# Kernel tuning notes

Measured on AMD Instinct MI355X. Metric: run time of the kernel, lower is better.

## Reference

```python
import math
import jax, jax.numpy as jnp
import numpy as np

B, C, H, W = 8, 512, 32, 32
HEADS = 8


def _mix_rot(re, im, Wm, phi):
    # nn.Linear(dim, dim, bias=False) applied channelwise on [B,C,H,W]:
    # y = x @ Wm.T  ->  einsum over input channel c, output channel d
    re2 = jnp.einsum('bchw,dc->bdhw', re, Wm)
    im2 = jnp.einsum('bchw,dc->bdhw', im, Wm)
    c = jnp.cos(phi)[None, :, None, None]
    s = jnp.sin(phi)[None, :, None, None]
    # complex multiply (re2 + i*im2) * (cos phi + i*sin phi)
    return re2 * c - im2 * s, re2 * s + im2 * c


def setup_inputs() -> dict:
    key = jax.random.key(0)
    ks = jax.random.split(key, 6)
    scale = 1.0 / math.sqrt(C)
    return {
        'z_re': jax.random.normal(ks[0], (B, C, H, W), jnp.float32),
        'z_im': jax.random.normal(ks[1], (B, C, H, W), jnp.float32),
        'Wq': jax.random.normal(ks[2], (C, C), jnp.float32) * scale,
        'phi_q': jnp.zeros((C,), jnp.float32),
        'Wk': jax.random.normal(ks[3], (C, C), jnp.float32) * scale,
        'phi_k': jnp.zeros((C,), jnp.float32),
        'Wv': jax.random.normal(ks[4], (C, C), jnp.float32) * scale,
        'phi_v': jnp.zeros((C,), jnp.float32),
        'Wo': jax.random.normal(ks[5], (C, C), jnp.float32) * scale,
        'phi_o': jnp.zeros((C,), jnp.float32),
    }


def reference(z_re, z_im, Wq, phi_q, Wk, phi_k, Wv, phi_v, Wo, phi_o):
    b, c, h, w = z_re.shape
    T = h * w
    dh = c // HEADS

    def tok(a):  # [B,C,H,W] -> [B,T,C]
        return a.reshape(b, c, T).transpose(0, 2, 1)

    qre, qim = _mix_rot(z_re, z_im, Wq, phi_q)
    kre, kim = _mix_rot(z_re, z_im, Wk, phi_k)
    vre, vim = _mix_rot(z_re, z_im, Wv, phi_v)
    qre, qim = tok(qre), tok(qim)
    kre, kim = tok(kre), tok(kim)
    vre, vim = tok(vre), tok(vim)

    # real part of complex inner product: sums over FULL channel dim (no head split)
    scores = (jnp.einsum('btc,buc->btu', qre, kre)
              + jnp.einsum('btc,buc->btu', qim, kim)) / math.sqrt(dh)
    causal = jnp.triu(jnp.ones((T, T), bool), k=1)
    scores = jnp.where(causal[None], -jnp.inf, scores)
    attn = jax.nn.softmax(scores, axis=-1)

    out_re = jnp.einsum('btu,buc->btc', attn, vre)
    out_im = jnp.einsum('btu,buc->btc', attn, vim)

    def grid(a):  # [B,T,C] -> [B,C,H,W]
        return a.transpose(0, 2, 1).reshape(b, c, h, w)

    return _mix_rot(grid(out_re), grid(out_im), Wo, phi_o)
```

## Files before the change

kernel.cpp:

```cpp
#include <hip/hip_runtime.h>
#include <math.h>

#define NB 8
#define NC 512
#define NT 1024
#define BT (NB * NT)
#define SCALE 0.125f
#define NEG_BIG (-3.0e38f)

typedef __attribute__((ext_vector_type(8))) short short8v;
typedef __attribute__((ext_vector_type(8))) _Float16 half8v;
typedef __attribute__((ext_vector_type(4))) float float4v;
#define MFMA_BF16(A, B, C) __builtin_amdgcn_mfma_f32_16x16x32_bf16(A, B, C, 0, 0, 0)
#define MFMA_F16(A, B, C)  __builtin_amdgcn_mfma_f32_16x16x32_f16(A, B, C, 0, 0, 0)

__device__ __forceinline__ ushort f2bf(float f) {
    union { float f; unsigned int i; } v; v.f = f;
    unsigned int r = v.i + 0x7FFFu + ((v.i >> 16) & 1u);
    return (ushort)(r >> 16);
}

__device__ __forceinline__ ushort f2h(float f) {
    return __builtin_bit_cast(unsigned short, (_Float16)f);
}

__device__ __forceinline__ half8v scale8(short8v raw, float s) {
    half8v h = __builtin_bit_cast(half8v, raw);
    const _Float16 hs = (_Float16)s;
    half8v r;
    #pragma unroll
    for (int q = 0; q < 8; ++q) r[q] = h[q] * hs;
    return r;
}

#if defined(__has_builtin)
#if __has_builtin(__builtin_amdgcn_global_load_lds)
#define HAS_GLDS 1
#endif
#endif

#ifdef HAS_GLDS
__device__ __forceinline__ void glds16(const ushort* g, ushort* l) {
    __builtin_amdgcn_global_load_lds(
        (const __attribute__((address_space(1))) unsigned int*)g,
        (__attribute__((address_space(3))) unsigned int*)l, 16, 0, 0);
}
#endif

template<int ROWS>
__device__ __forceinline__ void stage64(const ushort* __restrict__ g, int rsShorts,
                                        ushort* tile, int w, int lane) {
    const int r8 = lane >> 3;
    const int ck = (lane & 7) ^ r8;
    const ushort* gl = g + (size_t)r8 * rsShorts + (ck << 3);
    constexpr int ni = ROWS / 32;
    #pragma unroll
    for (int s = 0; s < ni; ++s) {
        const int issue = w * ni + s;
#ifdef HAS_GLDS
        glds16(gl + (size_t)issue * 8 * rsShorts, tile + issue * 512);
#else
        const uint4 v = *(const uint4*)(gl + (size_t)issue * 8 * rsShorts);
        *(uint4*)(tile + issue * 512 + lane * 8) = v;
#endif
    }
}

__device__ __forceinline__ short8v frag(const ushort* tile, int rr, int q) {
    return *(const short8v*)(tile + rr * 64 + ((q ^ (rr & 7)) << 3));
}

__device__ __forceinline__ int xcd_swz(int flat, int cpx) {
    return (flat & 7) * cpx + (flat >> 3);
}

__global__ __launch_bounds__(256) void prep_zw_kernel(
    const float* __restrict__ zre, const float* __restrict__ zim,
    ushort* __restrict__ Z,
    const float* __restrict__ Wq, const float* __restrict__ Wk,
    const float* __restrict__ Wv, const float* __restrict__ Wo,
    ushort* __restrict__ Wbf)
{
    const int bx = blockIdx.x;
    const int tid = threadIdx.x;
    if (bx >= 2048) {
        const int idx = (bx - 2048) * 256 + tid;
        const int e4 = idx << 2;
        const int m = e4 >> 18;
        const int off = e4 & ((1 << 18) - 1);
        const float* Ws[4] = {Wq, Wk, Wv, Wo};
        const float4 v = *(const float4*)(Ws[m] + off);
        ushort4 o;
        o.x = f2bf(v.x); o.y = f2bf(v.y); o.z = f2bf(v.z); o.w = f2bf(v.w);
        *(ushort4*)(Wbf + ((size_t)m << 18) + off) = o;
        return;
    }
    const int t0 = (bx & 15) << 6, c0 = ((bx >> 4) & 7) << 6;
    const int bz = bx >> 7, b = bz & 7, comp = bz >> 3;
    const float* src = (comp ? zim : zre) + (size_t)b * NC * NT;
    ushort* dst = Z + (size_t)(comp * NB + b) * NT * NC;

    __shared__ ushort T[64][72];
    #pragma unroll
    for (int r = 0; r < 4; ++r) {
        const int cl = (tid >> 4) + r * 16;
        const int t4 = (tid & 15) << 2;
        const float4 v = *(const float4*)(src + (size_t)(c0 + cl) * NT + t0 + t4);
        T[t4 + 0][cl] = f2bf(v.x); T[t4 + 1][cl] = f2bf(v.y);
        T[t4 + 2][cl] = f2bf(v.z); T[t4 + 3][cl] = f2bf(v.w);
    }
    __syncthreads();
    const int tl = tid >> 2, cc = (tid & 3) << 4;
    ushort* op = dst + (size_t)(t0 + tl) * NC + c0 + cc;
    *(uint4*)op       = *(const uint4*)&T[tl][cc];
    *(uint4*)(op + 8) = *(const uint4*)&T[tl][cc + 8];
}

__global__ __launch_bounds__(256, 2) void proj_qk_kernel(
    const ushort* __restrict__ Z, const ushort* __restrict__ Wbf,
    const float* __restrict__ phiq, const float* __restrict__ phik,
    ushort* __restrict__ qre, ushort* __restrict__ qim,
    ushort* __restrict__ kre, ushort* __restrict__ kim)
{
    const int tid = threadIdx.x;
    const int swz = xcd_swz(blockIdx.x + 64 * blockIdx.y, 64);
    const int d0 = (swz & 7) << 6;
    const int m0 = (swz >> 3) << 7;
    const size_t NE = (size_t)BT * NC;

    __shared__ alignas(16) ushort SM[24576];
    ushort* Zr   = SM;
    ushort* Zi   = SM + 8192;
    ushort* Wq_s = SM + 16384;
    ushort* Wk_s = SM + 20480;
    uint*   R    = (uint*)SM;

    float4v accq[2][4][2] = {};
    float4v acck[2][4][2] = {};

    const int w = tid >> 6, lane = tid & 63;
    const int l15 = lane & 15, quad = lane >> 4;
    const int wm = (w & 1) << 6;
    const int wn = (w >> 1) << 5;

    for (int c0 = 0; c0 < NC; c0 += 64) {
        stage64<128>(Z + (size_t)m0 * NC + c0, NC, Zr, w, lane);
        stage64<128>(Z + NE + (size_t)m0 * NC + c0, NC, Zi, w, lane);
        stage64<64>(Wbf + (size_t)d0 * NC + c0, NC, Wq_s, w, lane);
        stage64<64>(Wbf + ((size_t)1 << 18) + (size_t)d0 * NC + c0, NC, Wk_s, w, lane);
        __syncthreads();
        #pragma unroll
        for (int kk = 0; kk < 2; ++kk) {
            const int q0 = kk * 4 + quad;
            short8v zf[2][4], wqf[2], wkf[2];
            #pragma unroll
            for (int i = 0; i < 4; ++i) {
                zf[0][i] = frag(Zr, wm + i * 16 + l15, q0);
                zf[1][i] = frag(Zi, wm + i * 16 + l15, q0);
            }
            #pragma unroll
            for (int j = 0; j < 2; ++j) {
                wqf[j] = frag(Wq_s, wn + j * 16 + l15, q0);
                wkf[j] = frag(Wk_s, wn + j * 16 + l15, q0);
            }
            #pragma unroll
            for (int c = 0; c < 2; ++c)
                #pragma unroll
                for (int i = 0; i < 4; ++i)
                    #pragma unroll
                    for (int j = 0; j < 2; ++j) {
                        accq[c][i][j] = MFMA_BF16(zf[c][i], wqf[j], accq[c][i][j]);
                        acck[c][i][j] = MFMA_BF16(zf[c][i], wkf[j], acck[c][i][j]);
                    }
        }
        __syncthreads();
    }

    float cq[2], sq[2], ck2[2], sk2[2];
    #pragma unroll
    for (int j = 0; j < 2; ++j) {
        const int d = d0 + wn + j * 16 + l15;
        const float pq = phiq[d], pk = phik[d];
        cq[j] = cosf(pq); sq[j] = sinf(pq);
        ck2[j] = cosf(pk); sk2[j] = sinf(pk);
    }
    const int g = tid >> 4, cl = tid & 15;

    #pragma unroll
    for (int j = 0; j < 2; ++j)
        #pragma unroll
        for (int i = 0; i < 4; ++i)
            #pragma unroll
            for (int r = 0; r < 4; ++r) {
                const int row = wm + i * 16 + quad * 4 + r;
                const int col = wn + j * 16 + l15;
                const float ar = accq[0][i][j][r], ai = accq[1][i][j][r];
                R[row * 76 + col] = (uint)f2bf(ar * cq[j] - ai * sq[j])
                                  | ((uint)f2bf(ar * sq[j] + ai * cq[j]) << 16);
            }
    __syncthreads();
    #pragma unroll
    for (int s = 0; s < 8; ++s) {
        const int row = g * 8 + s;
        const uint4 p = *(const uint4*)&R[row * 76 + cl * 4];
        uint2 re, im;
        re.x = (p.x & 0xFFFFu) | (p.y << 16);
        re.y = (p.z & 0xFFFFu) | (p.w << 16);
        im.x = (p.x >> 16) | (p.y & 0xFFFF0000u);
        im.y = (p.z >> 16) | (p.w & 0xFFFF0000u);
        const size_t off = (size_t)(m0 + row) * NC + d0 + cl * 4;
        *(uint2*)(qre + off) = re;
        *(uint2*)(qim + off) = im;
    }
    __syncthreads();

    #pragma unroll
    for (int j = 0; j < 2; ++j)
        #pragma unroll
        for (int i = 0; i < 4; ++i)
            #pragma unroll
            for (int r = 0; r < 4; ++r) {
                const int row = wm + i * 16 + quad * 4 + r;
                const int col = wn + j * 16 + l15;
                const float br = acck[0][i][j][r], bi = acck[1][i][j][r];
                R[row * 76 + col] = (uint)f2bf(br * ck2[j] - bi * sk2[j])
                                  | ((uint)f2bf(br * sk2[j] + bi * ck2[j]) << 16);
            }
    __syncthreads();
    #pragma unroll
    for (int s = 0; s < 8; ++s) {
        const int row = g * 8 + s;
        const uint4 p = *(const uint4*)&R[row * 76 + cl * 4];
        uint2 re, im;
        re.x = (p.x & 0xFFFFu) | (p.y << 16);
        re.y = (p.z & 0xFFFFu) | (p.w << 16);
        im.x = (p.x >> 16) | (p.y & 0xFFFF0000u);
        im.y = (p.z >> 16) | (p.w & 0xFFFF0000u);
        const size_t off = (size_t)(m0 + row) * NC + d0 + cl * 4;
        *(uint2*)(kre + off) = re;
        *(uint2*)(kim + off) = im;
    }
}

__global__ __launch_bounds__(256, 3) void proj_v_kernel(
    const ushort* __restrict__ Z, const ushort* __restrict__ Wbf,
    const float* __restrict__ phiv,
    ushort* __restrict__ vre, ushort* __restrict__ vim)
{
    const int tid = threadIdx.x;
    const int swz = xcd_swz(blockIdx.x + 4 * blockIdx.y, 64);
    const int d0 = (swz & 3) << 7;
    const int bt0 = (swz >> 2) << 6;
    const size_t NE = (size_t)BT * NC;

    __shared__ alignas(16) ushort SM[19456];
    ushort* Wv_s = SM;
    ushort* Zr   = SM + 8192;
    ushort* Zi   = SM + 12288;
    uint*   R    = (uint*)SM;

    float4v acc[2][4][2] = {};

    const int w = tid >> 6, lane = tid & 63;
    const int l15 = lane & 15, quad = lane >> 4;
    const int wm = (w & 1) << 6;
    const int wn = (w >> 1) << 5;

    for (int c0 = 0; c0 < NC; c0 += 64) {
        stage64<128>(Wbf + ((size_t)2 << 18) + (size_t)d0 * NC + c0, NC, Wv_s, w, lane);
        stage64<64>(Z + (size_t)bt0 * NC + c0, NC, Zr, w, lane);
        stage64<64>(Z + NE + (size_t)bt0 * NC + c0, NC, Zi, w, lane);
        __syncthreads();
        #pragma unroll
        for (int kk = 0; kk < 2; ++kk) {
            const int q0 = kk * 4 + quad;
            short8v wvf[4], zf[2][2];
            #pragma unroll
            for (int i = 0; i < 4; ++i)
                wvf[i] = frag(Wv_s, wm + i * 16 + l15, q0);
            #pragma unroll
            for (int j = 0; j < 2; ++j) {
                zf[0][j] = frag(Zr, wn + j * 16 + l15, q0);
                zf[1][j] = frag(Zi, wn + j * 16 + l15, q0);
            }
            #pragma unroll
            for (int c = 0; c < 2; ++c)
                #pragma unroll
                for (int i = 0; i < 4; ++i)
                    #pragma unroll
                    for (int j = 0; j < 2; ++j)
                        acc[c][i][j] = MFMA_BF16(wvf[i], zf[c][j], acc[c][i][j]);
        }
        __syncthreads();
    }

    const int d_own = d0 + wm + (l15 >> 2) * 16 + quad * 4 + (l15 & 3);
    const float ph_own = phiv[d_own];
    const float c_own = cosf(ph_own), s_own = sinf(ph_own);

    #pragma unroll
    for (int i = 0; i < 4; ++i)
        #pragma unroll
        for (int r = 0; r < 4; ++r) {
            const int src = (lane & 48) | (i * 4 + r);
            const float cs = __shfl(c_own, src, 64);
            const float sn = __shfl(s_own, src, 64);
            const int row = wm + i * 16 + quad * 4 + r;
            #pragma unroll
            for (int j = 0; j < 2; ++j) {
                const int col = wn + j * 16 + l15;
                const float vr = acc[0][i][j][r], vi = acc[1][i][j][r];
                R[row * 76 + col] = (uint)f2h(vr * cs - vi * sn)
                                  | ((uint)f2h(vr * sn + vi * cs) << 16);
            }
        }
    __syncthreads();
    const int g = tid >> 4, cl = tid & 15;
    const int b = bt0 >> 10, t0 = bt0 & 1023;
    #pragma unroll
    for (int s = 0; s < 8; ++s) {
        const int row = g * 8 + s;
        const uint4 p = *(const uint4*)&R[row * 76 + cl * 4];
        uint2 re, im;
        re.x = (p.x & 0xFFFFu) | (p.y << 16);
        re.y = (p.z & 0xFFFFu) | (p.w << 16);
        im.x = (p.x >> 16) | (p.y & 0xFFFF0000u);
        im.y = (p.z >> 16) | (p.w & 0xFFFF0000u);
        const size_t off = (size_t)b * NC * NT + (size_t)(d0 + row) * NT + t0 + cl * 4;
        *(uint2*)(vre + off) = re;
        *(uint2*)(vim + off) = im;
    }
}

__global__ __launch_bounds__(256, 3) void scores_kernel(
    const ushort* __restrict__ qre, const ushort* __restrict__ qim,
    const ushort* __restrict__ kre, const ushort* __restrict__ kim,
    ushort* __restrict__ Pp, float2* __restrict__ stats)
{
    const int swz = xcd_swz(blockIdx.x + 8 * (blockIdx.y + 8 * blockIdx.z), 64);
    const int u0b = (swz & 7) << 7;
    const int t0b = (7 - ((swz >> 3) & 7)) << 7;
    if (u0b > t0b) return;
    const int b = swz >> 6;
    const int tid = threadIdx.x;
    const size_t qb = (size_t)b * NT * NC;

    __shared__ alignas(16) ushort SM[17920];
    ushort* Qs = SM;
    ushort* Ks = SM + 8192;
    ushort* Rs = SM;

    float4v acc[4][4] = {};

    const int w = tid >> 6, lane = tid & 63;
    const int l15 = lane & 15, quad = lane >> 4;
    const int wm = (w & 1) << 6;
    const int wn = (w >> 1) << 6;

    for (int c0 = 0; c0 < NC; c0 += 64) {
        stage64<128>(qre + qb + (size_t)t0b * NC + c0, NC, Qs, w, lane);
        stage64<128>(kre + qb + (size_t)u0b * NC + c0, NC, Ks, w, lane);
        __syncthreads();
        #pragma unroll
        for (int kk = 0; kk < 2; ++kk) {
            const int q0 = kk * 4 + quad;
            short8v qf[4], kf[4];
            #pragma unroll
            for (int i = 0; i < 4; ++i) {
                qf[i] = frag(Qs, wm + i * 16 + l15, q0);
                kf[i] = frag(Ks, wn + i * 16 + l15, q0);
            }
            #pragma unroll
            for (int i = 0; i < 4; ++i)
                #pragma unroll
                for (int j = 0; j < 4; ++j)
                    acc[i][j] = MFMA_BF16(qf[i], kf[j], acc[i][j]);
        }
        __syncthreads();
        stage64<128>(qim + qb + (size_t)t0b * NC + c0, NC, Qs, w, lane);
        stage64<128>(kim + qb + (size_t)u0b * NC + c0, NC, Ks, w, lane);
        __syncthreads();
        #pragma unroll
        for (int kk = 0; kk < 2; ++kk) {
            const int q0 = kk * 4 + quad;
            short8v qf[4], kf[4];
            #pragma unroll
            for (int i = 0; i < 4; ++i) {
                qf[i] = frag(Qs, wm + i * 16 + l15, q0);
                kf[i] = frag(Ks, wn + i * 16 + l15, q0);
            }
            #pragma unroll
            for (int i = 0; i < 4; ++i)
                #pragma unroll
                for (int j = 0; j < 4; ++j)
                    acc[i][j] = MFMA_BF16(qf[i], kf[j], acc[i][j]);
        }
        __syncthreads();
    }

    const int sub = (u0b + wn) >> 6;
    float2* st = stats + (size_t)(b * 16 + sub) * NT;
    #pragma unroll
    for (int i = 0; i < 4; ++i)
        #pragma unroll
        for (int r = 0; r < 4; ++r) {
            const int t = t0b + wm + i * 16 + quad * 4 + r;
            float v[4]; float m = NEG_BIG;
            #pragma unroll
            for (int j = 0; j < 4; ++j) {
                const int u = u0b + wn + j * 16 + l15;
                const float x = (u > t) ? NEG_BIG : acc[i][j][r] * SCALE;
                v[j] = x; m = fmaxf(m, x);
            }
            #pragma unroll
            for (int d = 1; d < 16; d <<= 1) m = fmaxf(m, __shfl_xor(m, d, 64));
            float l = 0.f;
            const int row = wm + i * 16 + quad * 4 + r;
            #pragma unroll
            for (int j = 0; j < 4; ++j) {
                const float e = __expf(v[j] - m);
                l += e;
                Rs[row * 140 + wn + j * 16 + l15] = f2h(e);
            }
            #pragma unroll
            for (int d = 1; d < 16; d <<= 1) l += __shfl_xor(l, d, 64);
            if (l15 == 0) st[t] = make_float2(m, l);
        }
    __syncthreads();
    ushort* Pb = Pp + (size_t)b * NT * NT;
    const int g = tid >> 5, cl = tid & 31;
    #pragma unroll
    for (int s = 0; s < 16; ++s) {
        const int row = g * 16 + s;
        const uint2 p = *(const uint2*)&Rs[row * 140 + cl * 4];
        *(uint2*)(Pb + (size_t)(t0b + row) * NT + u0b + cl * 4) = p;
    }
}

__global__ __launch_bounds__(256, 3) void pv_kernel(
    const ushort* __restrict__ Pp, const float2* __restrict__ stats,
    const ushort* __restrict__ vre, const ushort* __restrict__ vim,
    ushort* __restrict__ Ore, ushort* __restrict__ Oim)
{
    const int swz = xcd_swz(blockIdx.x + 8 * (blockIdx.y + 8 * blockIdx.z), 64);
    const int c0b = (swz & 7) << 6;
    const int t0b = (7 - ((swz >> 3) & 7)) << 7;
    const int b = swz >> 6;
    const int tid = threadIdx.x;
    const ushort* P = Pp + ((size_t)b * NT + t0b) * NT;
    const size_t vb = (size_t)b * NC * NT;
    const int iters = (t0b + 128) >> 6;

    __shared__ alignas(16) ushort SM[20736];
    ushort* Ps = SM;
    ushort* Vr = SM + 8192;
    ushort* Vi = SM + 12288;
    float* sLds = (float*)(SM + 16384);
    uint*  R    = (uint*)SM;

    float4v acc[2][4][2] = {};

    const int w = tid >> 6, lane = tid & 63;
    const int l15 = lane & 15, quad = lane >> 4;
    const int wm = (w & 1) << 6;
    const int wn = (w >> 1) << 5;

    if (tid < 128) {
        const int t = t0b + tid;
        float mv[16], lv[16];
        #pragma unroll
        for (int s = 0; s < 16; ++s) {
            if (s < iters) {
                const float2 v = stats[(size_t)(b * 16 + s) * NT + t];
                mv[s] = v.x; lv[s] = v.y;
            } else { mv[s] = NEG_BIG; lv[s] = 0.f; }
        }
        float M = NEG_BIG;
        #pragma unroll
        for (int s = 0; s < 16; ++s) M = fmaxf(M, mv[s]);
        float L = 0.f; float ev[16];
        #pragma unroll
        for (int s = 0; s < 16; ++s) { ev[s] = __expf(mv[s] - M); L += ev[s] * lv[s]; }
        const float inv = 1.0f / L;
        #pragma unroll
        for (int s = 0; s < 16; ++s) sLds[tid * 17 + s] = ev[s] * inv;
    }

    for (int it = 0; it < iters; ++it) {
        const int u0 = it << 6;
        stage64<128>(P + u0, NT, Ps, w, lane);
        stage64<64>(vre + vb + (size_t)c0b * NT + u0, NT, Vr, w, lane);
        stage64<64>(vim + vb + (size_t)c0b * NT + u0, NT, Vi, w, lane);
        __syncthreads();
        #pragma unroll
        for (int kk = 0; kk < 2; ++kk) {
            const int q0 = kk * 4 + quad;
            half8v pf[4], vf[2][2];
            #pragma unroll
            for (int i = 0; i < 4; ++i) {
                const int row = wm + i * 16 + l15;
                pf[i] = scale8(frag(Ps, row, q0), sLds[row * 17 + it]);
            }
            #pragma unroll
            for (int j = 0; j < 2; ++j) {
                vf[0][j] = __builtin_bit_cast(half8v, frag(Vr, wn + j * 16 + l15, q0));
                vf[1][j] = __builtin_bit_cast(half8v, frag(Vi, wn + j * 16 + l15, q0));
            }
            #pragma unroll
            for (int c = 0; c < 2; ++c)
                #pragma unroll
                for (int i = 0; i < 4; ++i)
                    #pragma unroll
                    for (int j = 0; j < 2; ++j)
                        acc[c][i][j] = MFMA_F16(pf[i], vf[c][j], acc[c][i][j]);
        }
        __syncthreads();
    }

    #pragma unroll
    for (int i = 0; i < 4; ++i)
        #pragma unroll
        for (int j = 0; j < 2; ++j)
            #pragma unroll
            for (int r = 0; r < 4; ++r) {
                const int row = wm + i * 16 + quad * 4 + r;
                const int col = wn + j * 16 + l15;
                R[row * 76 + col] = (uint)f2bf(acc[0][i][j][r])
                                  | ((uint)f2bf(acc[1][i][j][r]) << 16);
            }
    __syncthreads();
    const int g = tid >> 4, cl = tid & 15;
    #pragma unroll
    for (int s = 0; s < 8; ++s) {
        const int row = g * 8 + s;
        const uint4 p = *(const uint4*)&R[row * 76 + cl * 4];
        uint2 re, im;
        re.x = (p.x & 0xFFFFu) | (p.y << 16);
        re.y = (p.z & 0xFFFFu) | (p.w << 16);
        im.x = (p.x >> 16) | (p.y & 0xFFFF0000u);
        im.y = (p.z >> 16) | (p.w & 0xFFFF0000u);
        const size_t off = ((size_t)b * NT + t0b + row) * NC + c0b + cl * 4;
        *(uint2*)(Ore + off) = re;
        *(uint2*)(Oim + off) = im;
    }
}

__global__ __launch_bounds__(256, 3) void proj_out_kernel(
    const ushort* __restrict__ Ore, const ushort* __restrict__ Oim,
    const ushort* __restrict__ Wbf, const float* __restrict__ phio,
    float* __restrict__ outRe, float* __restrict__ outIm)
{
    const int tid = threadIdx.x;
    const int swz = xcd_swz(blockIdx.x + 4 * blockIdx.y, 64);
    const int d0 = (swz & 3) << 7;
    const int bt0 = (swz >> 2) << 6;

    __shared__ alignas(16) ushort SM[19456];
    ushort* Wo_s = SM;
    ushort* Or_s = SM + 8192;
    ushort* Oi_s = SM + 12288;
    float*  Rf   = (float*)SM;

    float4v acc[2][4][2] = {};

    const int w = tid >> 6, lane = tid & 63;
    const int l15 = lane & 15, quad = lane >> 4;
    const int wm = (w & 1) << 6;
    const int wn = (w >> 1) << 5;

    for (int c0 = 0; c0 < NC; c0 += 64) {
        stage64<128>(Wbf + ((size_t)3 << 18) + (size_t)d0 * NC + c0, NC, Wo_s, w, lane);
        stage64<64>(Ore + (size_t)bt0 * NC + c0, NC, Or_s, w, lane);
        stage64<64>(Oim + (size_t)bt0 * NC + c0, NC, Oi_s, w, lane);
        __syncthreads();
        #pragma unroll
        for (int kk = 0; kk < 2; ++kk) {
            const int q0 = kk * 4 + quad;
            short8v wof[4], of[2][2];
            #pragma unroll
            for (int i = 0; i < 4; ++i)
                wof[i] = frag(Wo_s, wm + i * 16 + l15, q0);
            #pragma unroll
            for (int j = 0; j < 2; ++j) {
                of[0][j] = frag(Or_s, wn + j * 16 + l15, q0);
                of[1][j] = frag(Oi_s, wn + j * 16 + l15, q0);
            }
            #pragma unroll
            for (int c = 0; c < 2; ++c)
                #pragma unroll
                for (int i = 0; i < 4; ++i)
                    #pragma unroll
                    for (int j = 0; j < 2; ++j)
                        acc[c][i][j] = MFMA_BF16(wof[i], of[c][j], acc[c][i][j]);
        }
        __syncthreads();
    }

    const int d_own = d0 + wm + (l15 >> 2) * 16 + quad * 4 + (l15 & 3);
    const float ph_own = phio[d_own];
    const float c_own = cosf(ph_own), s_own = sinf(ph_own);
    const int g = tid >> 4, cl = tid & 15;
    const int b = bt0 >> 10, t0 = bt0 & 1023;

    #pragma unroll
    for (int i = 0; i < 4; ++i)
        #pragma unroll
        for (int r = 0; r < 4; ++r) {
            const int src = (lane & 48) | (i * 4 + r);
            const float cs = __shfl(c_own, src, 64);
            const float sn = __shfl(s_own, src, 64);
            const int row = wm + i * 16 + quad * 4 + r;
            #pragma unroll
            for (int j = 0; j < 2; ++j) {
                const int col = wn + j * 16 + l15;
                Rf[row * 76 + col] = acc[0][i][j][r] * cs - acc[1][i][j][r] * sn;
            }
        }
    __syncthreads();
    #pragma unroll
    for (int s = 0; s < 8; ++s) {
        const int row = g * 8 + s;
        const float4 p = *(const float4*)&Rf[row * 76 + cl * 4];
        *(float4*)(outRe + (size_t)b * NC * NT + (size_t)(d0 + row) * NT + t0 + cl * 4) = p;
    }
    __syncthreads();

    #pragma unroll
    for (int i = 0; i < 4; ++i)
        #pragma unroll
        for (int r = 0; r < 4; ++r) {
            const int src = (lane & 48) | (i * 4 + r);
            const float cs = __shfl(c_own, src, 64);
            const float sn = __shfl(s_own, src, 64);
            const int row = wm + i * 16 + quad * 4 + r;
            #pragma unroll
            for (int j = 0; j < 2; ++j) {
                const int col = wn + j * 16 + l15;
                Rf[row * 76 + col] = acc[0][i][j][r] * sn + acc[1][i][j][r] * cs;
            }
        }
    __syncthreads();
    #pragma unroll
    for (int s = 0; s < 8; ++s) {
        const int row = g * 8 + s;
        const float4 p = *(const float4*)&Rf[row * 76 + cl * 4];
        *(float4*)(outIm + (size_t)b * NC * NT + (size_t)(d0 + row) * NT + t0 + cl * 4) = p;
    }
}

extern "C" void kernel_launch(void* const* d_in, const int* in_sizes, int n_in,
                              void* d_out, int out_size, void* d_ws, size_t ws_size,
                              hipStream_t stream) {
    (void)in_sizes; (void)n_in; (void)out_size; (void)ws_size;
    const float* z_re  = (const float*)d_in[0];
    const float* z_im  = (const float*)d_in[1];
    const float* Wq    = (const float*)d_in[2];
    const float* phi_q = (const float*)d_in[3];
    const float* Wk    = (const float*)d_in[4];
    const float* phi_k = (const float*)d_in[5];
    const float* Wv    = (const float*)d_in[6];
    const float* phi_v = (const float*)d_in[7];
    const float* Wo    = (const float*)d_in[8];
    const float* phi_o = (const float*)d_in[9];

    const size_t NE = (size_t)BT * NC;
    ushort* ws  = (ushort*)d_ws;
    ushort* qre = ws + 0 * NE; ushort* qim = ws + 1 * NE;
    ushort* kre = ws + 2 * NE; ushort* kim = ws + 3 * NE;
    ushort* vre = ws + 4 * NE; ushort* vim = ws + 5 * NE;
    ushort* Wbf = ws + 6 * NE;
    ushort* Z  = (ushort*)d_out;
    ushort* Pp = (ushort*)d_out + 2 * NE;
    float2* stats = (float2*)d_out;

    const dim3 blk(256);
    hipLaunchKernelGGL(prep_zw_kernel, dim3(3072), blk, 0, stream,
                       z_re, z_im, Z, Wq, Wk, Wv, Wo, Wbf);
    hipLaunchKernelGGL(proj_qk_kernel, dim3(BT / 128, NC / 64), blk, 0, stream,
                       Z, Wbf, phi_q, phi_k, qre, qim, kre, kim);
    hipLaunchKernelGGL(proj_v_kernel, dim3(NC / 128, BT / 64), blk, 0, stream,
                       Z, Wbf, phi_v, vre, vim);
    hipLaunchKernelGGL(scores_kernel, dim3(NT / 128, NT / 128, NB), blk, 0, stream,
                       qre, qim, kre, kim, Pp, stats);
    hipLaunchKernelGGL(pv_kernel, dim3(NC / 64, NT / 128, NB), blk, 0, stream,
                       Pp, stats, vre, vim, qre, qim);
    hipLaunchKernelGGL(proj_out_kernel, dim3(NC / 128, BT / 64), blk, 0, stream,
                       qre, qim, Wbf, phi_o, (float*)d_out, (float*)d_out + NE);
}
```

Before: 196.9 us.

## Load PV operands directly from global memory instead of staging through LDS

The PV kernel no longer stages P and V tiles into shared memory with barriers each iteration. Each lane now reads its MFMA fragments straight from global memory as 16-byte vector loads, and LDS is kept only for the softmax rescale factors and the output transpose. This removes per-iteration LDS writes, reads and two barriers, and shrinks LDS use, which may allow more occupancy. In exchange, operands shared across waves are fetched redundantly from L2/global memory, with no software prefetch to hide the latency.

```diff
diff --git a/kernel.cpp b/kernel.cpp
--- a/kernel.cpp
+++ b/kernel.cpp
@@ -447,16 +447,14 @@
     const int t0b = (7 - ((swz >> 3) & 7)) << 7;
     const int b = swz >> 6;
     const int tid = threadIdx.x;
-    const ushort* P = Pp + ((size_t)b * NT + t0b) * NT;
-    const size_t vb = (size_t)b * NC * NT;
+    const ushort* P  = Pp + ((size_t)b * NT + t0b) * NT;
+    const ushort* Vr = vre + (size_t)b * NC * NT + (size_t)c0b * NT;
+    const ushort* Vi = vim + (size_t)b * NC * NT + (size_t)c0b * NT;
     const int iters = (t0b + 128) >> 6;
 
-    __shared__ alignas(16) ushort SM[20736];
-    ushort* Ps = SM;
-    ushort* Vr = SM + 8192;
-    ushort* Vi = SM + 12288;
-    float* sLds = (float*)(SM + 16384);
-    uint*  R    = (uint*)SM;
+    __shared__ alignas(16) uint SMu[128 * 76];
+    float* sLds = (float*)SMu;
+    uint*  R    = SMu;
 
     float4v acc[2][4][2] = {};
 
@@ -485,38 +483,37 @@
         #pragma unroll
         for (int s = 0; s < 16; ++s) sLds[tid * 17 + s] = ev[s] * inv;
     }
+    __syncthreads();
 
     for (int it = 0; it < iters; ++it) {
         const int u0 = it << 6;
-        stage64<128>(P + u0, NT, Ps, w, lane);
-        stage64<64>(vre + vb + (size_t)c0b * NT + u0, NT, Vr, w, lane);
-        stage64<64>(vim + vb + (size_t)c0b * NT + u0, NT, Vi, w, lane);
-        __syncthreads();
         #pragma unroll
         for (int kk = 0; kk < 2; ++kk) {
-            const int q0 = kk * 4 + quad;
-            half8v pf[4], vf[2][2];
+            const int co = u0 + (kk * 4 + quad) * 8;
+            half8v pf[4], vfr[2], vfi[2];
             #pragma unroll
             for (int i = 0; i < 4; ++i) {
                 const int row = wm + i * 16 + l15;
-                pf[i] = scale8(frag(Ps, row, q0), sLds[row * 17 + it]);
+                const short8v raw = *(const short8v*)(P + (size_t)row * NT + co);
+                pf[i] = scale8(raw, sLds[row * 17 + it]);
             }
             #pragma unroll
             for (int j = 0; j < 2; ++j) {
-                vf[0][j] = __builtin_bit_cast(half8v, frag(Vr, wn + j * 16 + l15, q0));
-                vf[1][j] = __builtin_bit_cast(half8v, frag(Vi, wn + j * 16 + l15, q0));
-            }
-            #pragma unroll
-            for (int c = 0; c < 2; ++c)
+                const int cr = wn + j * 16 + l15;
+                vfr[j] = *(const half8v*)(Vr + (size_t)cr * NT + co);
+                vfi[j] = *(const half8v*)(Vi + (size_t)cr * NT + co);
+            }
+            #pragma unroll
+            for (int i = 0; i < 4; ++i)
                 #pragma unroll
-                for (int i = 0; i < 4; ++i)
-                    #pragma unroll
-                    for (int j = 0; j < 2; ++j)
-                        acc[c][i][j] = MFMA_F16(pf[i], vf[c][j], acc[c][i][j]);
-        }
-        __syncthreads();
-    }
-
+                for (int j = 0; j < 2; ++j) {
+                    acc[0][i][j] = MFMA_F16(pf[i], vfr[j], acc[0][i][j]);
+                    acc[1][i][j] = MFMA_F16(pf[i], vfi[j], acc[1][i][j]);
+                }
+        }
+    }
+
+    __syncthreads();
     #pragma unroll
     for (int i = 0; i < 4; ++i)
         #pragma unroll
```

Measured after the change: 228.1 us. 1.16x slower.
